# Optimization experiments

Measured on AMD Instinct MI355X. Metric: run time of the kernel, lower is better.

## Reference

```python
import jax, jax.numpy as jnp
import numpy as np

B, C, H, W = 16, 256, 48, 48
QD, KD, VD = 64, 64, 256


def setup_inputs() -> dict:
    key = jax.random.key(0)
    ks = jax.random.split(key, 6)
    s = 0.02
    return {
        "x": jax.random.normal(ks[0], (B, C, H, W), dtype=jnp.float32),
        "Wq": jax.random.normal(ks[1], (QD, C), dtype=jnp.float32) * s,
        "bq": jnp.zeros((QD,), dtype=jnp.float32),
        "Wk": jax.random.normal(ks[2], (KD, C), dtype=jnp.float32) * s,
        "bk": jnp.zeros((KD,), dtype=jnp.float32),
        "Wv": jax.random.normal(ks[3], (VD, C), dtype=jnp.float32) * s,
        "bv": jnp.zeros((VD,), dtype=jnp.float32),
        "Wo": jax.random.normal(ks[4], (C, VD), dtype=jnp.float32) * s,
        "bo": jnp.zeros((C,), dtype=jnp.float32),
        # torch init is gamma=0 (identity residual); use 0.5 so output/grads are non-trivial
        "gamma": jnp.full((1,), 0.5, dtype=jnp.float32),
    }


def reference(x, Wq, bq, Wk, bk, Wv, bv, Wo, bo, gamma):
    b, c, h, w = x.shape
    n = h * w
    xf = x.reshape(b, c, n)  # [B,C,N]
    # 1x1 convs == per-pixel channel matmuls
    q = jnp.einsum('oc,bcn->bon', Wq, xf) + bq[None, :, None]  # [B,QD,N]
    k = jnp.einsum('oc,bcn->bon', Wk, xf) + bk[None, :, None]  # [B,KD,N]
    # energy[b,i,j] = <q[:,i], k[:,j]>  (no scaling in original)
    energy = jnp.einsum('bqi,bqj->bij', q, k)  # [B,N,N]
    attention = jax.nn.softmax(energy, axis=-1)
    v = jnp.einsum('oc,bcn->bon', Wv, xf) + bv[None, :, None]  # [B,VD,N]
    # out = bmm(value, attention^T): out[:, :, i] = sum_j v[:, :, j] * attn[i, j]
    o = jnp.einsum('bvj,bij->bvi', v, attention)  # [B,VD,N]
    o = jnp.einsum('oc,bcn->bon', Wo, o) + bo[None, :, None]  # [B,C,N]
    out = gamma[0] * o.reshape(b, c, h, w) + x
    return out, attention
```

## Files before the change

kernel.cpp:

```cpp
#include <hip/hip_runtime.h>

#define B_ 16
#define C_ 256
#define N_ 2304
#define QD_ 64
#define VD_ 256

typedef unsigned short u16;
typedef __attribute__((ext_vector_type(8))) short bf16x8;
typedef __attribute__((ext_vector_type(4))) float f32x4;
typedef __attribute__((ext_vector_type(4))) u16 u16x4;

__device__ inline u16 f2b(float f){
  unsigned u = __builtin_bit_cast(unsigned, f);
  return (u16)((u + 0x7FFFu + ((u >> 16) & 1u)) >> 16);
}

__global__ void prep_weights(const float* __restrict__ Wq, const float* __restrict__ Wk,
                             const float* __restrict__ Wv, const float* __restrict__ Wo,
                             u16* __restrict__ W_all, u16* __restrict__ Wo_bf){
  int i = blockIdx.x * 256 + threadIdx.x;
  int row = i >> 8;
  float val;
  if (row < 64) val = Wq[i];
  else if (row < 128) val = Wk[i - 64*C_];
  else val = Wv[i - 128*C_];
  W_all[i] = f2b(val);
  if (i < C_*VD_) Wo_bf[i] = f2b(Wo[i]);
}

__global__ void transpose_x(const float* __restrict__ x, u16* __restrict__ x_t){
  __shared__ float tile[64][65];
  int b = blockIdx.z;
  int c0 = blockIdx.y * 64, n0 = blockIdx.x * 64;
  int tx = threadIdx.x & 63, ty = threadIdx.x >> 6;
  const float* xb = x + (size_t)b * C_ * N_;
  #pragma unroll
  for (int rr = 0; rr < 16; ++rr){
    int c = ty*16 + rr;
    tile[c][tx] = xb[(size_t)(c0 + c) * N_ + n0 + tx];
  }
  __syncthreads();
  u16* xtb = x_t + (size_t)b * N_ * C_;
  #pragma unroll
  for (int rr = 0; rr < 16; ++rr){
    int n = ty*16 + rr;
    xtb[(size_t)(n0 + n) * C_ + c0 + tx] = f2b(tile[tx][n]);
  }
}

template<int KD>
__device__ inline void mfma_tile64(const u16* __restrict__ A, const u16* __restrict__ Bt,
                                   f32x4 acc[4][4], int lane){
  int cl = lane & 15, q = lane >> 4;
  const u16* ab = A + cl*KD + q*8;
  const u16* bb = Bt + cl*KD + q*8;
  for (int kk = 0; kk < KD/32; ++kk){
    bf16x8 a[4], bfr[4];
    #pragma unroll
    for (int t = 0; t < 4; ++t) a[t] = *(const bf16x8*)(ab + t*16*KD + kk*32);
    #pragma unroll
    for (int t = 0; t < 4; ++t) bfr[t] = *(const bf16x8*)(bb + t*16*KD + kk*32);
    #pragma unroll
    for (int tm = 0; tm < 4; ++tm)
      #pragma unroll
      for (int tn = 0; tn < 4; ++tn)
        acc[tm][tn] = __builtin_amdgcn_mfma_f32_16x16x32_bf16(a[tm], bfr[tn], acc[tm][tn], 0, 0, 0);
  }
}

__global__ __launch_bounds__(512) void qkv_gemm(const u16* __restrict__ W_all, const u16* __restrict__ x_t,
    const float* __restrict__ bq, const float* __restrict__ bk, const float* __restrict__ bv,
    u16* __restrict__ q_t, u16* __restrict__ k_t, u16* __restrict__ v){
  int b = blockIdx.z;
  int lane = threadIdx.x & 63, wid = threadIdx.x >> 6;
  int m0 = blockIdx.x*128 + (wid >> 2)*64;
  int n0 = blockIdx.y*256 + (wid & 3)*64;
  const u16* xtb = x_t + (size_t)b*N_*C_;
  f32x4 acc[4][4] = {};
  mfma_tile64<C_>(W_all + (size_t)m0*C_, xtb + (size_t)n0*C_, acc, lane);
  int cl = lane & 15, q = lane >> 4;
  size_t qb = (size_t)b*N_*QD_;
  u16* vb = v + (size_t)b*VD_*N_;
  #pragma unroll
  for (int tm = 0; tm < 4; ++tm){
    int m = m0 + tm*16 + q*4;
    #pragma unroll
    for (int tn = 0; tn < 4; ++tn){
      int n = n0 + tn*16 + cl;
      f32x4 d = acc[tm][tn];
      if (m0 < 64){
        u16x4 pk;
        #pragma unroll
        for (int r = 0; r < 4; ++r) pk[r] = f2b(d[r] + bq[m + r]);
        *(u16x4*)(q_t + qb + (size_t)n*QD_ + m) = pk;
      } else if (m0 < 128){
        u16x4 pk;
        #pragma unroll
        for (int r = 0; r < 4; ++r) pk[r] = f2b(d[r] + bk[m - 64 + r]);
        *(u16x4*)(k_t + qb + (size_t)n*QD_ + (m - 64)) = pk;
      } else {
        #pragma unroll
        for (int r = 0; r < 4; ++r) vb[(size_t)(m - 128 + r)*N_ + n] = f2b(d[r] + bv[m - 128 + r]);
      }
    }
  }
}

__global__ __launch_bounds__(512) void energy_gemm(const u16* __restrict__ q_t, const u16* __restrict__ k_t,
                                                   float* __restrict__ attn){
  int b = blockIdx.z;
  int lane = threadIdx.x & 63, wid = threadIdx.x >> 6;
  int i0 = blockIdx.x*128 + (wid >> 2)*64;
  int j0 = blockIdx.y*256 + (wid & 3)*64;
  size_t qb = (size_t)b*N_*QD_;
  f32x4 acc[4][4] = {};
  mfma_tile64<QD_>(q_t + qb + (size_t)i0*QD_, k_t + qb + (size_t)j0*QD_, acc, lane);
  float* ab = attn + (size_t)b*N_*N_;
  int cl = lane & 15, q = lane >> 4;
  #pragma unroll
  for (int tm = 0; tm < 4; ++tm){
    int i = i0 + tm*16 + q*4;
    #pragma unroll
    for (int tn = 0; tn < 4; ++tn){
      int j = j0 + tn*16 + cl;
      #pragma unroll
      for (int r = 0; r < 4; ++r) ab[(size_t)(i + r)*N_ + j] = acc[tm][tn][r];
    }
  }
}

__global__ __launch_bounds__(576) void softmax_rows(float* __restrict__ attn, u16* __restrict__ attn_bf){
  int i = blockIdx.x, b = blockIdx.y;
  size_t base = ((size_t)b*N_ + i)*N_;
  float* row = attn + base;
  u16* brow = attn_bf + base;
  int t = threadIdx.x;
  int lane = t & 63, wid = t >> 6;
  f32x4 v = *(const f32x4*)(row + t*4);
  float mx = fmaxf(fmaxf(v[0], v[1]), fmaxf(v[2], v[3]));
  #pragma unroll
  for (int off = 1; off < 64; off <<= 1) mx = fmaxf(mx, __shfl_xor(mx, off));
  __shared__ float redm[9], reds[9];
  if (lane == 0) redm[wid] = mx;
  __syncthreads();
  mx = redm[0];
  #pragma unroll
  for (int k = 1; k < 9; ++k) mx = fmaxf(mx, redm[k]);
  float s = 0.f;
  #pragma unroll
  for (int k = 0; k < 4; ++k){ v[k] = __expf(v[k] - mx); s += v[k]; }
  #pragma unroll
  for (int off = 1; off < 64; off <<= 1) s += __shfl_xor(s, off);
  if (lane == 0) reds[wid] = s;
  __syncthreads();
  s = reds[0];
  #pragma unroll
  for (int k = 1; k < 9; ++k) s += reds[k];
  float inv = 1.0f / s;
  u16x4 pk;
  #pragma unroll
  for (int k = 0; k < 4; ++k){ v[k] *= inv; pk[k] = f2b(v[k]); }
  *(f32x4*)(row + t*4) = v;
  *(u16x4*)(brow + t*4) = pk;
}

__global__ __launch_bounds__(256) void pv_gemm(const u16* __restrict__ attn_bf, const u16* __restrict__ v,
                                               u16* __restrict__ o_t){
  int b = blockIdx.z;
  int lane = threadIdx.x & 63, wid = threadIdx.x >> 6;
  int i0 = blockIdx.x*128 + (wid >> 1)*64;
  int vd0 = blockIdx.y*128 + (wid & 1)*64;
  const u16* ab = attn_bf + (size_t)b*N_*N_;
  const u16* vb = v + (size_t)b*VD_*N_;
  f32x4 acc[4][4] = {};
  mfma_tile64<N_>(ab + (size_t)i0*N_, vb + (size_t)vd0*N_, acc, lane);
  u16* ob = o_t + (size_t)b*N_*VD_;
  int cl = lane & 15, q = lane >> 4;
  #pragma unroll
  for (int tm = 0; tm < 4; ++tm){
    int i = i0 + tm*16 + q*4;
    #pragma unroll
    for (int tn = 0; tn < 4; ++tn){
      int vd = vd0 + tn*16 + cl;
      #pragma unroll
      for (int r = 0; r < 4; ++r) ob[(size_t)(i + r)*VD_ + vd] = f2b(acc[tm][tn][r]);
    }
  }
}

__global__ __launch_bounds__(512) void out_gemm(const u16* __restrict__ Wo_bf, const u16* __restrict__ o_t,
    const float* __restrict__ bo, const float* __restrict__ gamma,
    const float* __restrict__ x, float* __restrict__ out){
  int b = blockIdx.z;
  int lane = threadIdx.x & 63, wid = threadIdx.x >> 6;
  int c0 = blockIdx.x*128 + (wid >> 2)*64;
  int n0 = blockIdx.y*256 + (wid & 3)*64;
  f32x4 acc[4][4] = {};
  mfma_tile64<VD_>(Wo_bf + (size_t)c0*VD_, o_t + (size_t)b*N_*VD_ + (size_t)n0*VD_, acc, lane);
  float g = gamma[0];
  const float* xb = x + (size_t)b*C_*N_;
  float* ob = out + (size_t)b*C_*N_;
  int cl = lane & 15, q = lane >> 4;
  #pragma unroll
  for (int tm = 0; tm < 4; ++tm){
    int c = c0 + tm*16 + q*4;
    #pragma unroll
    for (int tn = 0; tn < 4; ++tn){
      int n = n0 + tn*16 + cl;
      #pragma unroll
      for (int r = 0; r < 4; ++r){
        size_t idx = (size_t)(c + r)*N_ + n;
        ob[idx] = g*(acc[tm][tn][r] + bo[c + r]) + xb[idx];
      }
    }
  }
}

extern "C" void kernel_launch(void* const* d_in, const int* in_sizes, int n_in,
                              void* d_out, int out_size, void* d_ws, size_t ws_size,
                              hipStream_t stream){
  const float* x     = (const float*)d_in[0];
  const float* Wq    = (const float*)d_in[1];
  const float* bq    = (const float*)d_in[2];
  const float* Wk    = (const float*)d_in[3];
  const float* bk    = (const float*)d_in[4];
  const float* Wv    = (const float*)d_in[5];
  const float* bv    = (const float*)d_in[6];
  const float* Wo    = (const float*)d_in[7];
  const float* bo    = (const float*)d_in[8];
  const float* gamma = (const float*)d_in[9];

  float* out  = (float*)d_out;
  float* attn = out + (size_t)B_*C_*N_;

  char* ws = (char*)d_ws;
  u16* W_all   = (u16*)(ws + 0);
  u16* Wo_bf   = (u16*)(ws + 196608);
  u16* x_t     = (u16*)(ws + 327680);
  u16* q_t     = (u16*)(ws + 19202048);
  u16* k_t     = (u16*)(ws + 23920640);
  u16* v       = (u16*)(ws + 28639232);
  u16* o_t     = (u16*)(ws + 47513600);
  u16* attn_bf = (u16*)(ws + 66387968);

  prep_weights<<<dim3(384), 256, 0, stream>>>(Wq, Wk, Wv, Wo, W_all, Wo_bf);
  transpose_x<<<dim3(36, 4, 16), 256, 0, stream>>>(x, x_t);
  qkv_gemm<<<dim3(3, 9, 16), 512, 0, stream>>>(W_all, x_t, bq, bk, bv, q_t, k_t, v);
  energy_gemm<<<dim3(18, 9, 16), 512, 0, stream>>>(q_t, k_t, attn);
  softmax_rows<<<dim3(2304, 16), 576, 0, stream>>>(attn, attn_bf);
  pv_gemm<<<dim3(18, 2, 16), 256, 0, stream>>>(attn_bf, v, o_t);
  out_gemm<<<dim3(2, 9, 16), 512, 0, stream>>>(Wo_bf, o_t, bo, gamma, x, out);
}
```

Before: 878.2 us.

## Fuse energy GEMM and softmax with online two-pass recompute

Replaces the separate energy GEMM and row softmax kernels with one kernel per 64-row block. A first pass computes QK^T tiles and keeps running max and sum per row; a second pass recomputes the scores and writes the normalized fp32 and bf16 attention directly. This avoids writing the fp32 energy matrix and reading it back, at the cost of doing the QK^T matmul twice. The grid shrinks to 576 blocks, which may lower occupancy, and the stores are strided by row rather than fully coalesced.

```diff
diff --git a/kernel.cpp b/kernel.cpp
--- a/kernel.cpp
+++ b/kernel.cpp
@@ -107,62 +107,114 @@
   }
 }
 
-__global__ __launch_bounds__(512) void energy_gemm(const u16* __restrict__ q_t, const u16* __restrict__ k_t,
-                                                   float* __restrict__ attn){
-  int b = blockIdx.z;
-  int lane = threadIdx.x & 63, wid = threadIdx.x >> 6;
-  int i0 = blockIdx.x*128 + (wid >> 2)*64;
-  int j0 = blockIdx.y*256 + (wid & 3)*64;
+__global__ __launch_bounds__(512) void energy_softmax(const u16* __restrict__ q_t,
+    const u16* __restrict__ k_t, float* __restrict__ attn, u16* __restrict__ attn_bf){
+  int b = blockIdx.y;
+  int i0 = blockIdx.x * 64;
+  int lane = threadIdx.x & 63, w = threadIdx.x >> 6;
+  int cl = lane & 15, q = lane >> 4;
   size_t qb = (size_t)b*N_*QD_;
-  f32x4 acc[4][4] = {};
-  mfma_tile64<QD_>(q_t + qb + (size_t)i0*QD_, k_t + qb + (size_t)j0*QD_, acc, lane);
-  float* ab = attn + (size_t)b*N_*N_;
-  int cl = lane & 15, q = lane >> 4;
-  #pragma unroll
-  for (int tm = 0; tm < 4; ++tm){
-    int i = i0 + tm*16 + q*4;
-    #pragma unroll
-    for (int tn = 0; tn < 4; ++tn){
-      int j = j0 + tn*16 + cl;
-      #pragma unroll
-      for (int r = 0; r < 4; ++r) ab[(size_t)(i + r)*N_ + j] = acc[tm][tn][r];
-    }
-  }
-}
-
-__global__ __launch_bounds__(576) void softmax_rows(float* __restrict__ attn, u16* __restrict__ attn_bf){
-  int i = blockIdx.x, b = blockIdx.y;
-  size_t base = ((size_t)b*N_ + i)*N_;
-  float* row = attn + base;
-  u16* brow = attn_bf + base;
-  int t = threadIdx.x;
-  int lane = t & 63, wid = t >> 6;
-  f32x4 v = *(const f32x4*)(row + t*4);
-  float mx = fmaxf(fmaxf(v[0], v[1]), fmaxf(v[2], v[3]));
-  #pragma unroll
-  for (int off = 1; off < 64; off <<= 1) mx = fmaxf(mx, __shfl_xor(mx, off));
-  __shared__ float redm[9], reds[9];
-  if (lane == 0) redm[wid] = mx;
+  const u16* qbase = q_t + qb + (size_t)i0*QD_ + cl*QD_ + q*8;
+  const u16* kbase = k_t + qb + cl*QD_ + q*8;
+
+  bf16x8 af[4][2];
+  #pragma unroll
+  for (int t = 0; t < 4; ++t)
+    #pragma unroll
+    for (int kk = 0; kk < 2; ++kk)
+      af[t][kk] = *(const bf16x8*)(qbase + t*16*QD_ + kk*32);
+
+  float m_run[16], l_run[16];
+  #pragma unroll
+  for (int idx = 0; idx < 16; ++idx){ m_run[idx] = -3.0e38f; l_run[idx] = 0.f; }
+
+  for (int jt = w; jt < N_/64; jt += 8){
+    const u16* kb = kbase + (size_t)jt*64*QD_;
+    f32x4 acc[4][4] = {};
+    #pragma unroll
+    for (int kk = 0; kk < 2; ++kk){
+      bf16x8 bfr[4];
+      #pragma unroll
+      for (int t = 0; t < 4; ++t) bfr[t] = *(const bf16x8*)(kb + t*16*QD_ + kk*32);
+      #pragma unroll
+      for (int tm = 0; tm < 4; ++tm)
+        #pragma unroll
+        for (int tn = 0; tn < 4; ++tn)
+          acc[tm][tn] = __builtin_amdgcn_mfma_f32_16x16x32_bf16(af[tm][kk], bfr[tn], acc[tm][tn], 0, 0, 0);
+    }
+    #pragma unroll
+    for (int tm = 0; tm < 4; ++tm)
+      #pragma unroll
+      for (int r = 0; r < 4; ++r){
+        int idx = tm*4 + r;
+        float mt = fmaxf(fmaxf(acc[tm][0][r], acc[tm][1][r]), fmaxf(acc[tm][2][r], acc[tm][3][r]));
+        #pragma unroll
+        for (int mask = 1; mask < 16; mask <<= 1) mt = fmaxf(mt, __shfl_xor(mt, mask));
+        float mn = fmaxf(m_run[idx], mt);
+        float st = 0.f;
+        #pragma unroll
+        for (int tn = 0; tn < 4; ++tn) st += __expf(acc[tm][tn][r] - mn);
+        #pragma unroll
+        for (int mask = 1; mask < 16; mask <<= 1) st += __shfl_xor(st, mask);
+        l_run[idx] = l_run[idx]*__expf(m_run[idx] - mn) + st;
+        m_run[idx] = mn;
+      }
+  }
+
+  __shared__ float pm[8][64], pl[8][64];
+  if (cl == 0){
+    #pragma unroll
+    for (int idx = 0; idx < 16; ++idx){
+      int row = (idx >> 2)*16 + q*4 + (idx & 3);
+      pm[w][row] = m_run[idx];
+      pl[w][row] = l_run[idx];
+    }
+  }
   __syncthreads();
-  mx = redm[0];
-  #pragma unroll
-  for (int k = 1; k < 9; ++k) mx = fmaxf(mx, redm[k]);
-  float s = 0.f;
-  #pragma unroll
-  for (int k = 0; k < 4; ++k){ v[k] = __expf(v[k] - mx); s += v[k]; }
-  #pragma unroll
-  for (int off = 1; off < 64; off <<= 1) s += __shfl_xor(s, off);
-  if (lane == 0) reds[wid] = s;
-  __syncthreads();
-  s = reds[0];
-  #pragma unroll
-  for (int k = 1; k < 9; ++k) s += reds[k];
-  float inv = 1.0f / s;
-  u16x4 pk;
-  #pragma unroll
-  for (int k = 0; k < 4; ++k){ v[k] *= inv; pk[k] = f2b(v[k]); }
-  *(f32x4*)(row + t*4) = v;
-  *(u16x4*)(brow + t*4) = pk;
+  float M[16], invL[16];
+  #pragma unroll
+  for (int idx = 0; idx < 16; ++idx){
+    int row = (idx >> 2)*16 + q*4 + (idx & 3);
+    float mm = pm[0][row];
+    #pragma unroll
+    for (int ww = 1; ww < 8; ++ww) mm = fmaxf(mm, pm[ww][row]);
+    float L = 0.f;
+    #pragma unroll
+    for (int ww = 0; ww < 8; ++ww) L += pl[ww][row]*__expf(pm[ww][row] - mm);
+    M[idx] = mm;
+    invL[idx] = 1.0f / L;
+  }
+
+  float* arow = attn + (size_t)b*N_*N_ + (size_t)i0*N_;
+  u16* brow = attn_bf + (size_t)b*N_*N_ + (size_t)i0*N_;
+  for (int jt = w; jt < N_/64; jt += 8){
+    int j0 = jt*64;
+    const u16* kb = kbase + (size_t)jt*64*QD_;
+    f32x4 acc[4][4] = {};
+    #pragma unroll
+    for (int kk = 0; kk < 2; ++kk){
+      bf16x8 bfr[4];
+      #pragma unroll
+      for (int t = 0; t < 4; ++t) bfr[t] = *(const bf16x8*)(kb + t*16*QD_ + kk*32);
+      #pragma unroll
+      for (int tm = 0; tm < 4; ++tm)
+        #pragma unroll
+        for (int tn = 0; tn < 4; ++tn)
+          acc[tm][tn] = __builtin_amdgcn_mfma_f32_16x16x32_bf16(af[tm][kk], bfr[tn], acc[tm][tn], 0, 0, 0);
+    }
+    #pragma unroll
+    for (int tm = 0; tm < 4; ++tm)
+      #pragma unroll
+      for (int tn = 0; tn < 4; ++tn)
+        #pragma unroll
+        for (int r = 0; r < 4; ++r){
+          int idx = tm*4 + r;
+          float p = __expf(acc[tm][tn][r] - M[idx]) * invL[idx];
+          size_t off = (size_t)(tm*16 + q*4 + r)*N_ + j0 + tn*16 + cl;
+          arow[off] = p;
+          brow[off] = f2b(p);
+        }
+  }
 }
 
 __global__ __launch_bounds__(256) void pv_gemm(const u16* __restrict__ attn_bf, const u16* __restrict__ v,
@@ -247,8 +299,7 @@
   prep_weights<<<dim3(384), 256, 0, stream>>>(Wq, Wk, Wv, Wo, W_all, Wo_bf);
   transpose_x<<<dim3(36, 4, 16), 256, 0, stream>>>(x, x_t);
   qkv_gemm<<<dim3(3, 9, 16), 512, 0, stream>>>(W_all, x_t, bq, bk, bv, q_t, k_t, v);
-  energy_gemm<<<dim3(18, 9, 16), 512, 0, stream>>>(q_t, k_t, attn);
-  softmax_rows<<<dim3(2304, 16), 576, 0, stream>>>(attn, attn_bf);
+  energy_softmax<<<dim3(36, 16), 512, 0, stream>>>(q_t, k_t, attn, attn_bf);
   pv_gemm<<<dim3(18, 2, 16), 256, 0, stream>>>(attn_bf, v, o_t);
   out_gemm<<<dim3(2, 9, 16), 512, 0, stream>>>(Wo_bf, o_t, bo, gamma, x, out);
 }
```

After: 872.4 us. About the same (-0.7%).
